# Kernel tuning notes

Measured on AMD Instinct MI355X. Metric: run time of the kernel, lower is better.

## Reference

```python
import jax, jax.numpy as jnp
import numpy as np

K = 3            # kernel_size
PAD = K // 2
E = K * K        # num_elements

def setup_inputs() -> dict:
    key = jax.random.key(0)
    k1, k2, k3 = jax.random.split(key, 3)
    B, H, W, C = 8, 224, 224, 32
    inp = jax.random.uniform(k1, (B, H, W, C), dtype=jnp.float32)
    kernel = 0.5 + 0.05 * jax.random.uniform(k2, (E, 1, 1, 1, C), dtype=jnp.float32)
    mask = 0.75 + 0.05 * jax.random.uniform(k3, (E, 1, 1, 1, C), dtype=jnp.float32)
    return {"inp": inp, "kernel": kernel, "mask": mask}

def _shifted_stack(inp):
    # Replicates the TF loop ordering: element 0 is the unshifted input (center
    # tap), then taps in (y, x) raster order skipping the center.
    B, H, W, C = inp.shape
    padded = jnp.pad(inp, ((0, 0), (PAD, PAD), (PAD, PAD), (0, 0)))
    taps = [inp]
    for y in range(K):
        for x in range(K):
            if y != PAD or x != PAD:
                taps.append(padded[:, y:y + H, x:x + W, :])
    return jnp.stack(taps, axis=0)  # [E, B, H, W, C]

def reference(inp, kernel, mask):
    shifted = _shifted_stack(inp)                                   # [E,B,H,W,C]
    m = jnp.abs(mask) / (jnp.max(jnp.abs(mask)) + 1e-6)             # [E,1,1,1,C]
    sm = shifted * m                                                # masked taps
    diff = sm - kernel
    abs_diff = jnp.abs(diff)
    norm_1 = jnp.sum(abs_diff, axis=0)                              # [B,H,W,C]
    mean_diff = jnp.mean(diff, axis=0)                              # [B,H,W,C]
    variation_diff = jnp.sum(jnp.abs(abs_diff - mean_diff), axis=0) # [B,H,W,C]
    return (1.0 - variation_diff / E) * (1.0 - norm_1 / E)
```

## Files before the change

### kernel.cpp

```cpp
#include <hip/hip_runtime.h>

#define E  9
#define B_ 8
#define H_ 224
#define W_ 224
#define C_ 32
#define TH 4
#define TW 4
#define WT 32
#define STRIPS (H_ / TH)
#define WTILES (W_ / WT)
#define NBLK (B_ * STRIPS * WTILES)

__global__ __launch_bounds__(256) void fm_main(const float* __restrict__ inp,
                                               const float* __restrict__ kern,
                                               const float* __restrict__ mask,
                                               float* __restrict__ out) {
    int t = threadIdx.x;

    int bid = blockIdx.x;
    int swz = (bid & 7) * (NBLK / 8) + (bid >> 3);
    int bw  = swz % WTILES;
    int t2  = swz / WTILES;
    int hs  = (t2 % STRIPS) * TH;
    int b   = t2 / STRIPS;

    int c  = t & 31;
    int wg = t >> 5;
    int w0 = bw * WT + wg * TW;

    const float* base = inp + (((size_t)b * H_ * W_ + w0) * C_) + c;
    bool wm = (w0 > 0);
    bool wp = (w0 + TW < W_);

    float tap[TH + 2][TW + 2];
#pragma unroll
    for (int r = 0; r < TH + 2; ++r) {
        int hh = hs - 1 + r;
        if ((unsigned)hh < (unsigned)H_) {
            const float* p = base + (size_t)hh * (W_ * C_);
            tap[r][0] = wm ? p[-C_] : 0.f;
#pragma unroll
            for (int j = 1; j <= TW; ++j)
                tap[r][j] = p[(j - 1) * C_];
            tap[r][TW + 1] = wp ? p[TW * C_] : 0.f;
        } else {
#pragma unroll
            for (int j = 0; j < TW + 2; ++j) tap[r][j] = 0.f;
        }
    }

    float mv[E];
    float mx = 0.f;
#pragma unroll
    for (int e = 0; e < E; ++e) {
        mv[e] = fabsf(mask[e * C_ + c]);
        mx = fmaxf(mx, mv[e]);
    }
    mx = fmaxf(mx, __shfl_xor(mx, 1));
    mx = fmaxf(mx, __shfl_xor(mx, 2));
    mx = fmaxf(mx, __shfl_xor(mx, 4));
    mx = fmaxf(mx, __shfl_xor(mx, 8));
    mx = fmaxf(mx, __shfl_xor(mx, 16));
    float inv = 1.f / (mx + 1e-6f);

    float cm[E], ck[E];
#pragma unroll
    for (int e = 0; e < E; ++e) {
        cm[e] = mv[e] * inv;
        ck[e] = kern[e * C_ + c];
    }

    const int dyA[E] = {0, -1, -1, -1, 0, 0, 1, 1, 1};
    const int dxA[E] = {0, -1,  0,  1, -1, 1, -1, 0, 1};

    const float inv9 = 1.f / 9.f;

    float n[TH][TW], sm[TH][TW];
#pragma unroll
    for (int s = 0; s < TH; ++s)
#pragma unroll
        for (int j = 0; j < TW; ++j) { n[s][j] = 0.f; sm[s][j] = 0.f; }

#pragma unroll
    for (int e = 0; e < E; ++e) {
        float m = cm[e], k = ck[e];
#pragma unroll
        for (int s = 0; s < TH; ++s) {
#pragma unroll
            for (int j = 0; j < TW; ++j) {
                float d0 = fmaf(tap[s + 1 + dyA[e]][1 + j + dxA[e]], m, -k);
                n[s][j]  += fabsf(d0);
                sm[s][j] += d0;
            }
        }
    }

#pragma unroll
    for (int s = 0; s < TH; ++s) {
#pragma unroll
        for (int j = 0; j < TW; ++j) {
            float nm = sm[s][j] * (-inv9);
            float v = 0.f;
#pragma unroll
            for (int e = 0; e < E; ++e) {
                float d0 = fmaf(tap[s + 1 + dyA[e]][1 + j + dxA[e]],
                                cm[e], -ck[e]);
                v += fabsf(fabsf(d0) + nm);
            }
            float o = fmaf(v, -inv9, 1.f) * fmaf(n[s][j], -inv9, 1.f);

            float* op = out + (((size_t)b * H_ + (hs + s)) * W_ + (w0 + j)) * C_ + c;
            __builtin_nontemporal_store(o, op);
        }
    }
}

extern "C" void kernel_launch(void* const* d_in, const int* in_sizes, int n_in,
                              void* d_out, int out_size, void* d_ws, size_t ws_size,
                              hipStream_t stream) {
    const float* inp  = (const float*)d_in[0];
    const float* kern = (const float*)d_in[1];
    const float* mask = (const float*)d_in[2];
    float* out = (float*)d_out;

    fm_main<<<NBLK, 256, 0, stream>>>(inp, kern, mask, out);
}
```

Baseline: 25.40 us.

## Process two vertically stacked 7-row subtiles per thread, reusing halo rows

Reshapes each thread's tile from 4x4 outputs to two 7x2 subtiles stacked vertically. The two overlapping halo rows are carried over between subtiles rather than reloaded. This raises output per block and lowers the block count. Per-output load overhead stays about the same because the tiles are narrower, and there are fewer blocks to hide latency.

New measurement: 25.24 us. No clear change (-0.6%).

```diff
diff --git a/kernel.cpp b/kernel.cpp
--- a/kernel.cpp
+++ b/kernel.cpp
@@ -5,10 +5,11 @@
 #define H_ 224
 #define W_ 224
 #define C_ 32
-#define TH 4
-#define TW 4
-#define WT 32
-#define STRIPS (H_ / TH)
+#define TH 7
+#define NSUB 2
+#define TW 2
+#define WT 16
+#define STRIPS (H_ / (TH * NSUB))
 #define WTILES (W_ / WT)
 #define NBLK (B_ * STRIPS * WTILES)
 
@@ -22,7 +23,7 @@
     int swz = (bid & 7) * (NBLK / 8) + (bid >> 3);
     int bw  = swz % WTILES;
     int t2  = swz / WTILES;
-    int hs  = (t2 % STRIPS) * TH;
+    int hs  = (t2 % STRIPS) * (TH * NSUB);
     int b   = t2 / STRIPS;
 
     int c  = t & 31;
@@ -32,23 +33,6 @@
     const float* base = inp + (((size_t)b * H_ * W_ + w0) * C_) + c;
     bool wm = (w0 > 0);
     bool wp = (w0 + TW < W_);
-
-    float tap[TH + 2][TW + 2];
-#pragma unroll
-    for (int r = 0; r < TH + 2; ++r) {
-        int hh = hs - 1 + r;
-        if ((unsigned)hh < (unsigned)H_) {
-            const float* p = base + (size_t)hh * (W_ * C_);
-            tap[r][0] = wm ? p[-C_] : 0.f;
-#pragma unroll
-            for (int j = 1; j <= TW; ++j)
-                tap[r][j] = p[(j - 1) * C_];
-            tap[r][TW + 1] = wp ? p[TW * C_] : 0.f;
-        } else {
-#pragma unroll
-            for (int j = 0; j < TW + 2; ++j) tap[r][j] = 0.f;
-        }
-    }
 
     float mv[E];
     float mx = 0.f;
@@ -76,44 +60,75 @@
 
     const float inv9 = 1.f / 9.f;
 
-    float n[TH][TW], sm[TH][TW];
+    float tap[TH + 2][TW + 2];
+
+    auto ldrow = [&](int hh, float* r) {
+        if ((unsigned)hh < (unsigned)H_) {
+            const float* p = base + (size_t)hh * (W_ * C_);
+            r[0] = wm ? p[-C_] : 0.f;
+            r[1] = p[0];
+            r[2] = p[C_];
+            r[3] = wp ? p[2 * C_] : 0.f;
+        } else {
+            r[0] = 0.f; r[1] = 0.f; r[2] = 0.f; r[3] = 0.f;
+        }
+    };
+
+    auto process = [&](int rb) {
+        float n[TH][TW], sm[TH][TW];
 #pragma unroll
-    for (int s = 0; s < TH; ++s)
+        for (int s = 0; s < TH; ++s)
 #pragma unroll
-        for (int j = 0; j < TW; ++j) { n[s][j] = 0.f; sm[s][j] = 0.f; }
+            for (int j = 0; j < TW; ++j) { n[s][j] = 0.f; sm[s][j] = 0.f; }
 
 #pragma unroll
-    for (int e = 0; e < E; ++e) {
-        float m = cm[e], k = ck[e];
+        for (int e = 0; e < E; ++e) {
+            float m = cm[e], k = ck[e];
+#pragma unroll
+            for (int s = 0; s < TH; ++s) {
+#pragma unroll
+                for (int j = 0; j < TW; ++j) {
+                    float d0 = fmaf(tap[s + 1 + dyA[e]][1 + j + dxA[e]], m, -k);
+                    n[s][j]  += fabsf(d0);
+                    sm[s][j] += d0;
+                }
+            }
+        }
+
 #pragma unroll
         for (int s = 0; s < TH; ++s) {
 #pragma unroll
             for (int j = 0; j < TW; ++j) {
-                float d0 = fmaf(tap[s + 1 + dyA[e]][1 + j + dxA[e]], m, -k);
-                n[s][j]  += fabsf(d0);
-                sm[s][j] += d0;
+                float nm = sm[s][j] * (-inv9);
+                float v = 0.f;
+#pragma unroll
+                for (int e = 0; e < E; ++e) {
+                    float d0 = fmaf(tap[s + 1 + dyA[e]][1 + j + dxA[e]],
+                                    cm[e], -ck[e]);
+                    v += fabsf(fabsf(d0) + nm);
+                }
+                float o = fmaf(v, -inv9, 1.f) * fmaf(n[s][j], -inv9, 1.f);
+
+                float* op = out + (((size_t)b * H_ + (rb + s)) * W_ + (w0 + j)) * C_ + c;
+                __builtin_nontemporal_store(o, op);
             }
         }
-    }
+    };
 
 #pragma unroll
-    for (int s = 0; s < TH; ++s) {
+    for (int r = 0; r < TH + 2; ++r)
+        ldrow(hs - 1 + r, tap[r]);
+    process(hs);
+
 #pragma unroll
-        for (int j = 0; j < TW; ++j) {
-            float nm = sm[s][j] * (-inv9);
-            float v = 0.f;
+    for (int j = 0; j < TW + 2; ++j) {
+        tap[0][j] = tap[TH][j];
+        tap[1][j] = tap[TH + 1][j];
+    }
 #pragma unroll
-            for (int e = 0; e < E; ++e) {
-                float d0 = fmaf(tap[s + 1 + dyA[e]][1 + j + dxA[e]],
-                                cm[e], -ck[e]);
-                v += fabsf(fabsf(d0) + nm);
-            }
-            float o = fmaf(v, -inv9, 1.f) * fmaf(n[s][j], -inv9, 1.f);
-
-            float* op = out + (((size_t)b * H_ + (hs + s)) * W_ + (w0 + j)) * C_ + c;
-            __builtin_nontemporal_store(o, op);
-        }
-    }
+    for (int r = 2; r < TH + 2; ++r)
+        ldrow(hs + 6 + r, tap[r]);
+    process(hs + TH);
 }
 
 extern "C" void kernel_launch(void* const* d_in, const int* in_sizes, int n_in,
```
